# Performance work log

Measured on AMD Instinct MI355X. Metric: run time of the kernel, lower is better.

## Reference

```python
import jax, jax.numpy as jnp
import numpy as np

S, B, T, A = 512, 64, 768, 512
H1 = (T + T) // 2   # 768
H2 = (T + A) // 2   # 640


def setup_inputs() -> dict:
    key = jax.random.key(0)
    ks = jax.random.split(key, 11)
    sc = 0.02
    return {
        "text": jax.random.normal(ks[0], (B, T), jnp.float32),
        "anp": jax.random.normal(ks[1], (B, A), jnp.float32),
        "text_seq": jax.random.normal(ks[2], (S, B, T), jnp.float32),
        "W11": jax.random.normal(ks[3], (2 * T, H1), jnp.float32) * sc,
        "b11": jax.random.normal(ks[4], (H1,), jnp.float32) * sc,
        "W21": jax.random.normal(ks[5], (H1, 1), jnp.float32) * sc,
        "b21": jax.random.normal(ks[6], (1,), jnp.float32) * sc,
        "W12": jax.random.normal(ks[7], (T + A, H2), jnp.float32) * sc,
        "b12": jax.random.normal(ks[8], (H2,), jnp.float32) * sc,
        "W22": jax.random.normal(ks[9], (H2, 1), jnp.float32) * sc,
        "b22": jax.random.normal(ks[10], (1,), jnp.float32) * sc,
    }


def reference(text, anp, text_seq, W11, b11, W21, b21, W12, b12, W22, b22):
    t = text_seq.shape[-1]
    # cat([text_seq[i], text]) @ W11 == text_seq @ W11[:t] + text @ W11[t:]
    h1 = jnp.tanh(jnp.einsum("sbt,th->sbh", text_seq, W11[:t]) + text @ W11[t:] + b11)
    h2 = jnp.tanh(jnp.einsum("sbt,th->sbh", text_seq, W12[:t]) + anp @ W12[t:] + b12)
    s1 = h1 @ W21 + b21            # (S, B, 1)
    s2 = h2 @ W22 + b22            # (S, B, 1)
    w1 = jax.nn.softmax(s1, axis=0)
    w2 = jax.nn.softmax(s2, axis=0)
    return jnp.mean((w1 + w2) * text_seq * 0.5, axis=0)  # (B, T)
```

## Files before the change

### kernel.cpp

```cpp
#include <hip/hip_runtime.h>
#include <stdint.h>

#define S_DIM 512
#define B_DIM 64
#define T_DIM 768
#define A_DIM 512
#define H1_DIM 768
#define H2_DIM 640
#define N_DIM (H1_DIM + H2_DIM)
#define M_DIM (S_DIM * B_DIM)
#define K_DIM T_DIM

typedef short s16x8 __attribute__((ext_vector_type(8)));
typedef float f32x4 __attribute__((ext_vector_type(4)));

__device__ __forceinline__ unsigned short f2bf(float f) {
    unsigned u = __float_as_uint(f);
    u += 0x7fffu + ((u >> 16) & 1u);
    return (unsigned short)(u >> 16);
}

__global__ __launch_bounds__(256) void convA_kernel(const float* __restrict__ ts,
                                                    unsigned short* __restrict__ Abf) {
    int i = blockIdx.x * 256 + threadIdx.x;
    float4 v = ((const float4*)ts)[i];
    ushort4 o;
    o.x = f2bf(v.x); o.y = f2bf(v.y); o.z = f2bf(v.z); o.w = f2bf(v.w);
    ((ushort4*)Abf)[i] = o;
}

__global__ __launch_bounds__(256) void convW_kernel(const float* __restrict__ W11,
                                                    const float* __restrict__ W12,
                                                    unsigned short* __restrict__ Bt) {
    int e = blockIdx.x * 256 + threadIdx.x;
    int n = e / K_DIM, k = e % K_DIM;
    float v = (n < H1_DIM) ? W11[k * H1_DIM + n] : W12[k * H2_DIM + (n - H1_DIM)];
    Bt[e] = f2bf(v);
}

__global__ __launch_bounds__(256) void bias_kernel(const float* __restrict__ text,
                                                   const float* __restrict__ anp,
                                                   const float* __restrict__ W11,
                                                   const float* __restrict__ b11,
                                                   const float* __restrict__ W12,
                                                   const float* __restrict__ b12,
                                                   float* __restrict__ cbias) {
    int e = blockIdx.x * 256 + threadIdx.x;
    int b = e / N_DIM, n = e % N_DIM;
    float a0 = 0.f, a1 = 0.f, a2 = 0.f, a3 = 0.f, base;
    if (n < H1_DIM) {
        base = b11[n];
        const float* w = W11 + (size_t)T_DIM * H1_DIM + n;
        const float* x = text + b * T_DIM;
        for (int k = 0; k < T_DIM; k += 4) {
            a0 = fmaf(x[k],     w[(size_t)k * H1_DIM],       a0);
            a1 = fmaf(x[k + 1], w[(size_t)(k + 1) * H1_DIM], a1);
            a2 = fmaf(x[k + 2], w[(size_t)(k + 2) * H1_DIM], a2);
            a3 = fmaf(x[k + 3], w[(size_t)(k + 3) * H1_DIM], a3);
        }
    } else {
        int n2 = n - H1_DIM;
        base = b12[n2];
        const float* w = W12 + (size_t)T_DIM * H2_DIM + n2;
        const float* x = anp + b * A_DIM;
        for (int k = 0; k < A_DIM; k += 4) {
            a0 = fmaf(x[k],     w[(size_t)k * H2_DIM],       a0);
            a1 = fmaf(x[k + 1], w[(size_t)(k + 1) * H2_DIM], a1);
            a2 = fmaf(x[k + 2], w[(size_t)(k + 2) * H2_DIM], a2);
            a3 = fmaf(x[k + 3], w[(size_t)(k + 3) * H2_DIM], a3);
        }
    }
    cbias[e] = base + ((a0 + a1) + (a2 + a3));
}

#define BM 128
#define BN 128
#define BK 64

__global__ __launch_bounds__(256, 2) void gemm_score_kernel(
        const unsigned short* __restrict__ A,
        const unsigned short* __restrict__ Bt,
        const float* __restrict__ cbias,
        const float* __restrict__ W21,
        const float* __restrict__ W22,
        float* __restrict__ score) {
    __shared__ __align__(16) unsigned short As[BM * BK];
    __shared__ __align__(16) unsigned short Bs[BN * BK];
    const int tid  = threadIdx.x;
    const int m0   = blockIdx.x * BM;
    const int n0   = blockIdx.y * BN;
    const int lane = tid & 63;
    const int wave = tid >> 6;
    const int wm   = wave & 1;
    const int wn   = wave >> 1;
    const int quad = lane >> 4;
    const int col  = lane & 15;
    const int cswz = col & 7;

    f32x4 acc[4][4] = {};

    const int wrow = lane >> 3;
    const int kof  = (((lane & 7) ^ wrow) & 7) * 8;

    for (int k0 = 0; k0 < K_DIM; k0 += BK) {
        #pragma unroll
        for (int p = 0; p < 4; ++p) {
            const int r0 = p * 32 + wave * 8;
            __builtin_amdgcn_global_load_lds(
                (__attribute__((address_space(1))) void*)&A[(size_t)(m0 + r0 + wrow) * K_DIM + k0 + kof],
                (__attribute__((address_space(3))) void*)&As[r0 * BK],
                16, 0, 0);
            __builtin_amdgcn_global_load_lds(
                (__attribute__((address_space(1))) void*)&Bt[(size_t)(n0 + r0 + wrow) * K_DIM + k0 + kof],
                (__attribute__((address_space(3))) void*)&Bs[r0 * BK],
                16, 0, 0);
        }
        __syncthreads();
        #pragma unroll
        for (int kk = 0; kk < BK; kk += 32) {
            s16x8 af[4], bf[4];
            const int ch = ((kk >> 3) + quad) ^ cswz;
            #pragma unroll
            for (int i = 0; i < 4; ++i)
                af[i] = *(const s16x8*)&As[(wm * 64 + i * 16 + col) * BK + ch * 8];
            #pragma unroll
            for (int j = 0; j < 4; ++j)
                bf[j] = *(const s16x8*)&Bs[(wn * 64 + j * 16 + col) * BK + ch * 8];
            #pragma unroll
            for (int i = 0; i < 4; ++i)
                #pragma unroll
                for (int j = 0; j < 4; ++j)
                    acc[i][j] = __builtin_amdgcn_mfma_f32_16x16x32_bf16(af[i], bf[j], acc[i][j], 0, 0, 0);
        }
        __syncthreads();
    }

    const int half = (n0 >= H1_DIM) ? 1 : 0;
    const float* w2p = half ? (W22 - H1_DIM) : W21;
    int   ncol[4];
    float w2v[4];
    #pragma unroll
    for (int j = 0; j < 4; ++j) {
        ncol[j] = n0 + wn * 64 + j * 16 + col;
        w2v[j]  = w2p[ncol[j]];
    }
    float* sc = score + half * M_DIM;
    #pragma unroll
    for (int i = 0; i < 4; ++i) {
        #pragma unroll
        for (int r = 0; r < 4; ++r) {
            int row_local = wm * 64 + i * 16 + quad * 4 + r;
            int b = row_local & (B_DIM - 1);
            int s = (m0 + row_local) >> 6;
            float v = 0.f;
            #pragma unroll
            for (int j = 0; j < 4; ++j) {
                float pre = acc[i][j][r] + cbias[b * N_DIM + ncol[j]];
                float ex  = __expf(2.f * pre);
                float th  = 1.f - 2.f * __builtin_amdgcn_rcpf(ex + 1.f);
                v = fmaf(th, w2v[j], v);
            }
            v += __shfl_xor(v, 1);
            v += __shfl_xor(v, 2);
            v += __shfl_xor(v, 4);
            v += __shfl_xor(v, 8);
            if (col == 0) atomicAdd(&sc[b * S_DIM + s], v);
        }
    }
}

__global__ __launch_bounds__(512) void softmax_kernel(const float* __restrict__ score,
                                                      float* __restrict__ wsum) {
    const int b = blockIdx.x, s = threadIdx.x;
    __shared__ float redm[16], reds[16];
    float v0 = score[b * S_DIM + s];
    float v1 = score[M_DIM + b * S_DIM + s];
    float m0 = v0, m1 = v1;
    #pragma unroll
    for (int off = 32; off > 0; off >>= 1) {
        m0 = fmaxf(m0, __shfl_xor(m0, off));
        m1 = fmaxf(m1, __shfl_xor(m1, off));
    }
    const int w = s >> 6;
    if ((s & 63) == 0) { redm[w] = m0; redm[8 + w] = m1; }
    __syncthreads();
    m0 = redm[0]; m1 = redm[8];
    #pragma unroll
    for (int i = 1; i < 8; ++i) { m0 = fmaxf(m0, redm[i]); m1 = fmaxf(m1, redm[8 + i]); }
    float e0 = expf(v0 - m0), e1 = expf(v1 - m1);
    float s0 = e0, s1 = e1;
    #pragma unroll
    for (int off = 32; off > 0; off >>= 1) {
        s0 += __shfl_xor(s0, off);
        s1 += __shfl_xor(s1, off);
    }
    if ((s & 63) == 0) { reds[w] = s0; reds[8 + w] = s1; }
    __syncthreads();
    s0 = reds[0]; s1 = reds[8];
    #pragma unroll
    for (int i = 1; i < 8; ++i) { s0 += reds[i]; s1 += reds[8 + i]; }
    wsum[b * S_DIM + s] = e0 / s0 + e1 / s1;
}

__global__ __launch_bounds__(256) void wmean_kernel(const unsigned short* __restrict__ Abf,
                                                    const float* __restrict__ wsum,
                                                    float* __restrict__ out) {
    int e = blockIdx.x * 256 + threadIdx.x;
    int s0 = blockIdx.y * 64;
    int b = e / (T_DIM / 2), tp = e % (T_DIM / 2);
    const unsigned short* base = Abf + (size_t)b * T_DIM + tp * 2;
    float a0 = 0.f, a1 = 0.f, c0 = 0.f, c1 = 0.f;
    #pragma unroll 4
    for (int s = s0; s < s0 + 64; s += 2) {
        float w0 = wsum[b * S_DIM + s];
        float w1 = wsum[b * S_DIM + s + 1];
        unsigned u0 = *(const unsigned*)(base + (size_t)s * (B_DIM * T_DIM));
        unsigned u1 = *(const unsigned*)(base + (size_t)(s + 1) * (B_DIM * T_DIM));
        a0 = fmaf(w0, __uint_as_float(u0 << 16),          a0);
        a1 = fmaf(w0, __uint_as_float(u0 & 0xffff0000u),  a1);
        c0 = fmaf(w1, __uint_as_float(u1 << 16),          c0);
        c1 = fmaf(w1, __uint_as_float(u1 & 0xffff0000u),  c1);
    }
    atomicAdd(&out[b * T_DIM + tp * 2],     (a0 + c0) * (0.5f / (float)S_DIM));
    atomicAdd(&out[b * T_DIM + tp * 2 + 1], (a1 + c1) * (0.5f / (float)S_DIM));
}

extern "C" void kernel_launch(void* const* d_in, const int* in_sizes, int n_in,
                              void* d_out, int out_size, void* d_ws, size_t ws_size,
                              hipStream_t stream) {
    const float* text = (const float*)d_in[0];
    const float* anp  = (const float*)d_in[1];
    const float* ts   = (const float*)d_in[2];
    const float* W11  = (const float*)d_in[3];
    const float* b11  = (const float*)d_in[4];
    const float* W21  = (const float*)d_in[5];
    const float* W12  = (const float*)d_in[7];
    const float* b12  = (const float*)d_in[8];
    const float* W22  = (const float*)d_in[9];
    float* out = (float*)d_out;

    char* ws = (char*)d_ws;
    unsigned short* Abf = (unsigned short*)ws;
    unsigned short* Bt  = (unsigned short*)(ws + 50331648);
    float* cbias = (float*)(ws + 50331648 + 2162688);
    float* score = (float*)(ws + 50331648 + 2162688 + 360448);
    float* wsum  = (float*)(ws + 50331648 + 2162688 + 360448 + 262144);

    hipMemsetAsync(score, 0, 2 * M_DIM * sizeof(float), stream);
    hipMemsetAsync(out, 0, B_DIM * T_DIM * sizeof(float), stream);

    convA_kernel<<<M_DIM * K_DIM / 1024, 256, 0, stream>>>(ts, Abf);
    convW_kernel<<<N_DIM * K_DIM / 256, 256, 0, stream>>>(W11, W12, Bt);
    bias_kernel<<<B_DIM * N_DIM / 256, 256, 0, stream>>>(text, anp, W11, b11, W12, b12, cbias);
    gemm_score_kernel<<<dim3(M_DIM / BM, N_DIM / BN), 256, 0, stream>>>(Abf, Bt, cbias, W21, W22, score);
    softmax_kernel<<<B_DIM, 512, 0, stream>>>(score, wsum);
    wmean_kernel<<<dim3(B_DIM * T_DIM / 512, 8), 256, 0, stream>>>(Abf, wsum, out);
}
```

Before: 349.9 us.

## Merge prep kernels, replace atomics with partial buffers, drop memsets

Merges the three preprocessing kernels into one launch and removes both memsets. The GEMM epilogue now combines the two N-waves through shared memory and writes per-column-block partial scores instead of doing atomic adds, and the softmax sums the 11 partials. The grid is swapped so N blocks vary fastest, which may improve reuse of the A tile in L2. The weighted-mean kernel now loops over all S per thread and writes directly without atomics, which cuts its parallelism to 192 blocks of 128 threads. The GEMM epilogue also gains extra __syncthreads calls.

```diff
diff --git a/kernel.cpp b/kernel.cpp
--- a/kernel.cpp
+++ b/kernel.cpp
@@ -10,6 +10,7 @@
 #define N_DIM (H1_DIM + H2_DIM)
 #define M_DIM (S_DIM * B_DIM)
 #define K_DIM T_DIM
+#define NJB 11
 
 typedef short s16x8 __attribute__((ext_vector_type(8)));
 typedef float f32x4 __attribute__((ext_vector_type(4)));
@@ -20,57 +21,60 @@
     return (unsigned short)(u >> 16);
 }
 
-__global__ __launch_bounds__(256) void convA_kernel(const float* __restrict__ ts,
-                                                    unsigned short* __restrict__ Abf) {
-    int i = blockIdx.x * 256 + threadIdx.x;
-    float4 v = ((const float4*)ts)[i];
-    ushort4 o;
-    o.x = f2bf(v.x); o.y = f2bf(v.y); o.z = f2bf(v.z); o.w = f2bf(v.w);
-    ((ushort4*)Abf)[i] = o;
-}
-
-__global__ __launch_bounds__(256) void convW_kernel(const float* __restrict__ W11,
-                                                    const float* __restrict__ W12,
-                                                    unsigned short* __restrict__ Bt) {
-    int e = blockIdx.x * 256 + threadIdx.x;
-    int n = e / K_DIM, k = e % K_DIM;
-    float v = (n < H1_DIM) ? W11[k * H1_DIM + n] : W12[k * H2_DIM + (n - H1_DIM)];
-    Bt[e] = f2bf(v);
-}
-
-__global__ __launch_bounds__(256) void bias_kernel(const float* __restrict__ text,
+#define CONVA_BLKS (M_DIM * K_DIM / 1024)
+#define CONVW_BLKS (N_DIM * K_DIM / 256)
+#define BIAS_BLKS  (B_DIM * N_DIM / 256)
+
+__global__ __launch_bounds__(256) void prep_kernel(const float* __restrict__ ts,
+                                                   const float* __restrict__ text,
                                                    const float* __restrict__ anp,
                                                    const float* __restrict__ W11,
                                                    const float* __restrict__ b11,
                                                    const float* __restrict__ W12,
                                                    const float* __restrict__ b12,
+                                                   unsigned short* __restrict__ Abf,
+                                                   unsigned short* __restrict__ Bt,
                                                    float* __restrict__ cbias) {
-    int e = blockIdx.x * 256 + threadIdx.x;
-    int b = e / N_DIM, n = e % N_DIM;
-    float a0 = 0.f, a1 = 0.f, a2 = 0.f, a3 = 0.f, base;
-    if (n < H1_DIM) {
-        base = b11[n];
-        const float* w = W11 + (size_t)T_DIM * H1_DIM + n;
-        const float* x = text + b * T_DIM;
-        for (int k = 0; k < T_DIM; k += 4) {
-            a0 = fmaf(x[k],     w[(size_t)k * H1_DIM],       a0);
-            a1 = fmaf(x[k + 1], w[(size_t)(k + 1) * H1_DIM], a1);
-            a2 = fmaf(x[k + 2], w[(size_t)(k + 2) * H1_DIM], a2);
-            a3 = fmaf(x[k + 3], w[(size_t)(k + 3) * H1_DIM], a3);
-        }
+    const int blk = blockIdx.x;
+    if (blk < CONVA_BLKS) {
+        int i = blk * 256 + threadIdx.x;
+        float4 v = ((const float4*)ts)[i];
+        ushort4 o;
+        o.x = f2bf(v.x); o.y = f2bf(v.y); o.z = f2bf(v.z); o.w = f2bf(v.w);
+        ((ushort4*)Abf)[i] = o;
+    } else if (blk < CONVA_BLKS + CONVW_BLKS) {
+        int e = (blk - CONVA_BLKS) * 256 + threadIdx.x;
+        int n = e / K_DIM, k = e % K_DIM;
+        float v = (n < H1_DIM) ? W11[k * H1_DIM + n] : W12[k * H2_DIM + (n - H1_DIM)];
+        Bt[e] = f2bf(v);
     } else {
-        int n2 = n - H1_DIM;
-        base = b12[n2];
-        const float* w = W12 + (size_t)T_DIM * H2_DIM + n2;
-        const float* x = anp + b * A_DIM;
-        for (int k = 0; k < A_DIM; k += 4) {
-            a0 = fmaf(x[k],     w[(size_t)k * H2_DIM],       a0);
-            a1 = fmaf(x[k + 1], w[(size_t)(k + 1) * H2_DIM], a1);
-            a2 = fmaf(x[k + 2], w[(size_t)(k + 2) * H2_DIM], a2);
-            a3 = fmaf(x[k + 3], w[(size_t)(k + 3) * H2_DIM], a3);
-        }
-    }
-    cbias[e] = base + ((a0 + a1) + (a2 + a3));
+        int e = (blk - CONVA_BLKS - CONVW_BLKS) * 256 + threadIdx.x;
+        int b = e / N_DIM, n = e % N_DIM;
+        float a0 = 0.f, a1 = 0.f, a2 = 0.f, a3 = 0.f, base;
+        if (n < H1_DIM) {
+            base = b11[n];
+            const float* w = W11 + (size_t)T_DIM * H1_DIM + n;
+            const float* x = text + b * T_DIM;
+            for (int k = 0; k < T_DIM; k += 4) {
+                a0 = fmaf(x[k],     w[(size_t)k * H1_DIM],       a0);
+                a1 = fmaf(x[k + 1], w[(size_t)(k + 1) * H1_DIM], a1);
+                a2 = fmaf(x[k + 2], w[(size_t)(k + 2) * H1_DIM], a2);
+                a3 = fmaf(x[k + 3], w[(size_t)(k + 3) * H1_DIM], a3);
+            }
+        } else {
+            int n2 = n - H1_DIM;
+            base = b12[n2];
+            const float* w = W12 + (size_t)T_DIM * H2_DIM + n2;
+            const float* x = anp + b * A_DIM;
+            for (int k = 0; k < A_DIM; k += 4) {
+                a0 = fmaf(x[k],     w[(size_t)k * H2_DIM],       a0);
+                a1 = fmaf(x[k + 1], w[(size_t)(k + 1) * H2_DIM], a1);
+                a2 = fmaf(x[k + 2], w[(size_t)(k + 2) * H2_DIM], a2);
+                a3 = fmaf(x[k + 3], w[(size_t)(k + 3) * H2_DIM], a3);
+            }
+        }
+        cbias[e] = base + ((a0 + a1) + (a2 + a3));
+    }
 }
 
 #define BM 128
@@ -83,12 +87,12 @@
         const float* __restrict__ cbias,
         const float* __restrict__ W21,
         const float* __restrict__ W22,
-        float* __restrict__ score) {
+        float* __restrict__ part) {
     __shared__ __align__(16) unsigned short As[BM * BK];
     __shared__ __align__(16) unsigned short Bs[BN * BK];
     const int tid  = threadIdx.x;
-    const int m0   = blockIdx.x * BM;
-    const int n0   = blockIdx.y * BN;
+    const int n0   = blockIdx.x * BN;
+    const int m0   = blockIdx.y * BM;
     const int lane = tid & 63;
     const int wave = tid >> 6;
     const int wm   = wave & 1;
@@ -136,6 +140,7 @@
     }
 
     const int half = (n0 >= H1_DIM) ? 1 : 0;
+    const int jb   = half ? (6 + ((n0 - H1_DIM) >> 7)) : (n0 >> 7);
     const float* w2p = half ? (W22 - H1_DIM) : W21;
     int   ncol[4];
     float w2v[4];
@@ -144,7 +149,7 @@
         ncol[j] = n0 + wn * 64 + j * 16 + col;
         w2v[j]  = w2p[ncol[j]];
     }
-    float* sc = score + half * M_DIM;
+    float* pc = part + jb * M_DIM;
     #pragma unroll
     for (int i = 0; i < 4; ++i) {
         #pragma unroll
@@ -164,17 +169,25 @@
             v += __shfl_xor(v, 2);
             v += __shfl_xor(v, 4);
             v += __shfl_xor(v, 8);
-            if (col == 0) atomicAdd(&sc[b * S_DIM + s], v);
-        }
-    }
-}
-
-__global__ __launch_bounds__(512) void softmax_kernel(const float* __restrict__ score,
+            __syncthreads();
+            float* scr = (float*)As;
+            if (col == 0 && wn == 0) scr[row_local] = v;
+            __syncthreads();
+            if (col == 0 && wn == 1) pc[b * S_DIM + s] = v + scr[row_local];
+            __syncthreads();
+        }
+    }
+}
+
+__global__ __launch_bounds__(512) void softmax_kernel(const float* __restrict__ part,
                                                       float* __restrict__ wsum) {
     const int b = blockIdx.x, s = threadIdx.x;
     __shared__ float redm[16], reds[16];
-    float v0 = score[b * S_DIM + s];
-    float v1 = score[M_DIM + b * S_DIM + s];
+    float v0 = 0.f, v1 = 0.f;
+    #pragma unroll
+    for (int jb = 0; jb < 6; ++jb)  v0 += part[jb * M_DIM + b * S_DIM + s];
+    #pragma unroll
+    for (int jb = 6; jb < 11; ++jb) v1 += part[jb * M_DIM + b * S_DIM + s];
     float m0 = v0, m1 = v1;
     #pragma unroll
     for (int off = 32; off > 0; off >>= 1) {
@@ -202,18 +215,17 @@
     wsum[b * S_DIM + s] = e0 / s0 + e1 / s1;
 }
 
-__global__ __launch_bounds__(256) void wmean_kernel(const unsigned short* __restrict__ Abf,
+__global__ __launch_bounds__(128) void wmean_kernel(const unsigned short* __restrict__ Abf,
                                                     const float* __restrict__ wsum,
                                                     float* __restrict__ out) {
-    int e = blockIdx.x * 256 + threadIdx.x;
-    int s0 = blockIdx.y * 64;
-    int b = e / (T_DIM / 2), tp = e % (T_DIM / 2);
+    const int b  = blockIdx.x;
+    const int tp = blockIdx.y * 128 + threadIdx.x;
     const unsigned short* base = Abf + (size_t)b * T_DIM + tp * 2;
+    const float* wp = wsum + b * S_DIM;
     float a0 = 0.f, a1 = 0.f, c0 = 0.f, c1 = 0.f;
     #pragma unroll 4
-    for (int s = s0; s < s0 + 64; s += 2) {
-        float w0 = wsum[b * S_DIM + s];
-        float w1 = wsum[b * S_DIM + s + 1];
+    for (int s = 0; s < S_DIM; s += 2) {
+        float w0 = wp[s], w1 = wp[s + 1];
         unsigned u0 = *(const unsigned*)(base + (size_t)s * (B_DIM * T_DIM));
         unsigned u1 = *(const unsigned*)(base + (size_t)(s + 1) * (B_DIM * T_DIM));
         a0 = fmaf(w0, __uint_as_float(u0 << 16),          a0);
@@ -221,8 +233,8 @@
         c0 = fmaf(w1, __uint_as_float(u1 << 16),          c0);
         c1 = fmaf(w1, __uint_as_float(u1 & 0xffff0000u),  c1);
     }
-    atomicAdd(&out[b * T_DIM + tp * 2],     (a0 + c0) * (0.5f / (float)S_DIM));
-    atomicAdd(&out[b * T_DIM + tp * 2 + 1], (a1 + c1) * (0.5f / (float)S_DIM));
+    out[b * T_DIM + tp * 2]     = (a0 + c0) * (0.5f / (float)S_DIM);
+    out[b * T_DIM + tp * 2 + 1] = (a1 + c1) * (0.5f / (float)S_DIM);
 }
 
 extern "C" void kernel_launch(void* const* d_in, const int* in_sizes, int n_in,
@@ -243,16 +255,13 @@
     unsigned short* Abf = (unsigned short*)ws;
     unsigned short* Bt  = (unsigned short*)(ws + 50331648);
     float* cbias = (float*)(ws + 50331648 + 2162688);
-    float* score = (float*)(ws + 50331648 + 2162688 + 360448);
-    float* wsum  = (float*)(ws + 50331648 + 2162688 + 360448 + 262144);
-
-    hipMemsetAsync(score, 0, 2 * M_DIM * sizeof(float), stream);
-    hipMemsetAsync(out, 0, B_DIM * T_DIM * sizeof(float), stream);
-
-    convA_kernel<<<M_DIM * K_DIM / 1024, 256, 0, stream>>>(ts, Abf);
-    convW_kernel<<<N_DIM * K_DIM / 256, 256, 0, stream>>>(W11, W12, Bt);
-    bias_kernel<<<B_DIM * N_DIM / 256, 256, 0, stream>>>(text, anp, W11, b11, W12, b12, cbias);
-    gemm_score_kernel<<<dim3(M_DIM / BM, N_DIM / BN), 256, 0, stream>>>(Abf, Bt, cbias, W21, W22, score);
-    softmax_kernel<<<B_DIM, 512, 0, stream>>>(score, wsum);
-    wmean_kernel<<<dim3(B_DIM * T_DIM / 512, 8), 256, 0, stream>>>(Abf, wsum, out);
-}
+    float* part  = (float*)(ws + 50331648 + 2162688 + 360448);
+    float* wsum  = (float*)(ws + 50331648 + 2162688 + 360448 + 1441792);
+
+    prep_kernel<<<CONVA_BLKS + CONVW_BLKS + BIAS_BLKS, 256, 0, stream>>>(
+        ts, text, anp, W11, b11, W12, b12, Abf, Bt, cbias);
+    gemm_score_kernel<<<dim3(N_DIM / BN, M_DIM / BM), 256, 0, stream>>>(
+        Abf, Bt, cbias, W21, W22, part);
+    softmax_kernel<<<B_DIM, 512, 0, stream>>>(part, wsum);
+    wmean_kernel<<<dim3(B_DIM, 3), 128, 0, stream>>>(Abf, wsum, out);
+}
```

Result: slower. 364.8 us (+4.3%).
